# Performance work log

Hardware: AMD Instinct MI355X
Metric: run time of the kernel (lower is better)

## Reference

```python
import jax, jax.numpy as jnp
import numpy as np

B, CIN, COUT, H, W = 8, 256, 256, 64, 64


def setup_inputs() -> dict:
    key = jax.random.key(0)
    k1, k2, k3 = jax.random.split(key, 3)
    x = jax.random.normal(k1, (B, CIN, H, W), dtype=jnp.float32)
    style = jax.random.normal(k2, (B, CIN), dtype=jnp.float32)
    # kaiming_normal_ (fan_in = CIN*3*3, gain = sqrt(2))
    fan_in = CIN * 9
    weight = jax.random.normal(k3, (COUT, CIN, 3, 3), dtype=jnp.float32) * np.sqrt(2.0 / fan_in)
    return {"x": x, "style": style, "weight": weight}


def reference(x, style, weight):
    b, cin, h, w = x.shape
    cout = weight.shape[0]
    # modulate: [B, Cout, Cin, 3, 3]
    mw = style[:, None, :, None, None] * weight[None]
    # demodulate
    sigma = jnp.sqrt(jnp.sum(mw * mw, axis=(2, 3, 4), keepdims=True) + 1e-8)
    dw = mw / sigma
    # per-sample conv via grouped convolution (groups = B)
    x_g = x.reshape(1, b * cin, h, w)
    w_g = dw.reshape(b * cout, cin, 3, 3)
    out = jax.lax.conv_general_dilated(
        x_g, w_g,
        window_strides=(1, 1),
        padding=((1, 1), (1, 1)),
        feature_group_count=b,
        dimension_numbers=("NCHW", "OIHW", "NCHW"),
    )
    return out.reshape(b, cout, h, w)
```

## Files before the change

kernel.cpp:

```cpp
#include <hip/hip_runtime.h>

#define B_ 8
#define CIN_ 256
#define COUT_ 256

typedef short short8_t __attribute__((ext_vector_type(8)));
typedef float float16_t __attribute__((ext_vector_type(16)));

#define DWA_SHORTS   (B_ * 2 * 8 * 9 * 4 * 128 * 8)
#define XPRE_SHORTS  (B_ * 8 * 66 * 4 * 66 * 8)

__device__ __forceinline__ unsigned short f2bf(float f) {
    union { float f; unsigned u; } v; v.f = f;
    unsigned u = v.u;
    unsigned r = (u + 0x7fffu + ((u >> 16) & 1u)) >> 16;
    return (unsigned short)r;
}

__global__ __launch_bounds__(256) void k_prep(const float* __restrict__ x,
                                              const float* __restrict__ style,
                                              const float* __restrict__ weight,
                                              unsigned short* __restrict__ xpre,
                                              float* __restrict__ invp) {
    const int bid = blockIdx.x;
    const int t = threadIdx.x;

    if (bid < 4224) {
        const int h_out = bid % 66;
        const int t2 = bid / 66;
        const int cb = t2 & 7, b = t2 >> 3;
        const int h_in = h_out - 1;
        const int g = t >> 6, lane = t & 63;
        unsigned short* dst =
            xpre + (((size_t)(b * 8 + cb) * 66 + h_out) * 4 + g) * (66 * 8);
#pragma unroll
        for (int pass = 0; pass < 2; ++pass) {
            int w_out = pass * 64 + lane;
            if (pass == 1 && lane >= 2) break;
            int w_in = w_out - 1;
            short8_t v = (short8_t){0, 0, 0, 0, 0, 0, 0, 0};
            if ((unsigned)h_in < 64u && (unsigned)w_in < 64u) {
                const float* xp =
                    x + (((size_t)(b * CIN_ + cb * 32 + g * 8)) * 64 + h_in) * 64 + w_in;
#pragma unroll
                for (int j = 0; j < 8; ++j) v[j] = (short)f2bf(xp[(size_t)j * 4096]);
            }
            *(short8_t*)(dst + (size_t)w_out * 8) = v;
        }
    } else {
        const int co = (bid - 4224) * 16 + (t >> 4);
        const int sl = t & 15;
        float part[8];
#pragma unroll
        for (int b = 0; b < 8; ++b) part[b] = 0.f;
        const float* wr = weight + (size_t)co * 2304 + sl * 16 * 9;
#pragma unroll 4
        for (int k = 0; k < 16; ++k) {
            int ci = sl * 16 + k;
            float a = 0.f;
#pragma unroll
            for (int tp = 0; tp < 9; ++tp) { float w = wr[k * 9 + tp]; a += w * w; }
#pragma unroll
            for (int b = 0; b < 8; ++b) {
                float s = style[b * CIN_ + ci];
                part[b] += s * s * a;
            }
        }
#pragma unroll
        for (int b = 0; b < 8; ++b) {
            float p = part[b];
            p += __shfl_xor(p, 1, 64);
            p += __shfl_xor(p, 2, 64);
            p += __shfl_xor(p, 4, 64);
            p += __shfl_xor(p, 8, 64);
            if (sl == 0) invp[b * COUT_ + co] = 1.0f / sqrtf(p + 1e-8f);
        }
    }
}

__global__ __launch_bounds__(256) void k_wpack(const float* __restrict__ weight,
                                               const float* __restrict__ style,
                                               const float* __restrict__ invp,
                                               unsigned short* __restrict__ dwA) {
    const int co_blk = blockIdx.x, cb = blockIdx.y, b = blockIdx.z;
    const int t = threadIdx.x;
    unsigned short* slab = dwA + (((size_t)(b * 2 + co_blk) * 8 + cb) * 9) * 4096;
    const int co = co_blk * 128 + (t & 127);
    const float iv = invp[b * COUT_ + co];
    const float* wco = weight + (size_t)co * 2304;
#pragma unroll
    for (int i = 0; i < 18; ++i) {
        int o8 = t + i * 256;
        int g = (o8 >> 7) & 3;
        int tap = o8 >> 9;
        int ci0 = cb * 32 + g * 8;
        short8_t v;
#pragma unroll
        for (int k = 0; k < 8; ++k)
            v[k] = (short)f2bf(wco[(ci0 + k) * 9 + tap] * style[b * CIN_ + ci0 + k] * iv);
        *(short8_t*)(slab + (size_t)o8 * 8) = v;
    }
}

__global__ __launch_bounds__(256, 2) void k_conv(const unsigned short* __restrict__ xpre,
                                                 const unsigned short* __restrict__ dwA,
                                                 float* __restrict__ out) {
    __shared__ __align__(16) unsigned short xs[2][4 * 4 * 66 * 8];

    const int rowgrp = blockIdx.x;
    const int co_blk = blockIdx.y;
    const int b = blockIdx.z;
    const int tid = threadIdx.x;
    const int lane = tid & 63, wid = tid >> 6;
    const int wave_m = wid & 1;
    const int wave_r = wid >> 1;
    const int l32 = lane & 31, kh = lane >> 5;
    const int r0 = rowgrp * 2;

    float16_t acc[2][2];
#pragma unroll
    for (int mi = 0; mi < 2; ++mi)
#pragma unroll
        for (int nj = 0; nj < 2; ++nj)
#pragma unroll
            for (int r = 0; r < 16; ++r) acc[mi][nj][r] = 0.f;

    short8_t st[5];
    auto load_regs = [&](int cb) {
        const unsigned short* s =
            xpre + ((size_t)(b * 8 + cb) * 66 + r0) * (4 * 66 * 8);
#pragma unroll
        for (int it = 0; it < 4; ++it)
            st[it] = *(const short8_t*)(s + (size_t)(tid + it * 256) * 8);
        if (tid < 32) st[4] = *(const short8_t*)(s + (size_t)(tid + 1024) * 8);
    };
    auto store_lds = [&](int buf) {
        unsigned short* d = xs[buf];
#pragma unroll
        for (int it = 0; it < 4; ++it)
            *(short8_t*)(d + (size_t)(tid + it * 256) * 8) = st[it];
        if (tid < 32) *(short8_t*)(d + (size_t)(tid + 1024) * 8) = st[4];
    };

    short8_t abuf[3][4];
    auto loadA = [&](short8_t* dst, int acb, int atap) {
        const unsigned short* Ab =
            dwA + ((((size_t)(b * 2 + co_blk) * 8 + acb) * 9 + atap)) * 4096;
        const int co_off = wave_m * 64 + l32;
#pragma unroll
        for (int ks = 0; ks < 2; ++ks)
#pragma unroll
            for (int mi = 0; mi < 2; ++mi)
                dst[ks * 2 + mi] = *(const short8_t*)(
                    Ab + (size_t)((ks * 2 + kh) * 128 + co_off + mi * 32) * 8);
    };

    load_regs(0);
    loadA(abuf[0], 0, 0);
    loadA(abuf[1], 0, 1);

    for (int cb = 0; cb < 8; ++cb) {
        store_lds(cb & 1);
        __syncthreads();
        if (cb < 7) load_regs(cb + 1);

        const unsigned short* xb = xs[cb & 1];
#pragma unroll
        for (int tap = 0; tap < 9; ++tap) {
            const int nl = tap + 2;
            const int acb = cb + nl / 9, atap = nl % 9;
            if (acb < 8) loadA(abuf[(tap + 2) % 3], acb, atap);

            const int dh = tap / 3, dwc = tap - dh * 3;
            const unsigned short* bb =
                xb + (size_t)(((wave_r + dh) * 4 + kh) * 66 + l32 + dwc) * 8;
            short8_t bf[2][2];
#pragma unroll
            for (int ks = 0; ks < 2; ++ks)
#pragma unroll
                for (int nj = 0; nj < 2; ++nj)
                    bf[ks][nj] = *(const short8_t*)(bb + (size_t)(ks * 2 * 66 + nj * 32) * 8);

            const short8_t* ac = abuf[tap % 3];
#pragma unroll
            for (int ks = 0; ks < 2; ++ks)
#pragma unroll
                for (int mi = 0; mi < 2; ++mi)
#pragma unroll
                    for (int nj = 0; nj < 2; ++nj)
                        acc[mi][nj] = __builtin_amdgcn_mfma_f32_32x32x16_bf16(
                            ac[ks * 2 + mi], bf[ks][nj], acc[mi][nj], 0, 0, 0);
        }
    }

    const int orow = r0 + wave_r;
#pragma unroll
    for (int mi = 0; mi < 2; ++mi)
#pragma unroll
        for (int nj = 0; nj < 2; ++nj)
#pragma unroll
            for (int r = 0; r < 16; ++r) {
                int co = co_blk * 128 + wave_m * 64 + mi * 32 + (r & 3) + 8 * (r >> 2) + 4 * kh;
                int c = nj * 32 + l32;
                out[(((size_t)b * COUT_ + co) * 64 + orow) * 64 + c] = acc[mi][nj][r];
            }
}

extern "C" void kernel_launch(void* const* d_in, const int* in_sizes, int n_in,
                              void* d_out, int out_size, void* d_ws, size_t ws_size,
                              hipStream_t stream) {
    const float* x = (const float*)d_in[0];
    const float* style = (const float*)d_in[1];
    const float* weight = (const float*)d_in[2];
    float* out = (float*)d_out;

    unsigned short* dwA = (unsigned short*)d_ws;
    unsigned short* xpre = dwA + DWA_SHORTS;
    float* invp = (float*)(xpre + XPRE_SHORTS);

    k_prep<<<dim3(4240), 256, 0, stream>>>(x, style, weight, xpre, invp);
    k_wpack<<<dim3(2, 8, B_), 256, 0, stream>>>(weight, style, invp, dwA);
    k_conv<<<dim3(32, 2, B_), 256, 0, stream>>>(xpre, dwA, out);
}
```

Measured before the change: 152.8 us.

## Fuse demodulation into weight packing and shrink conv tile to one row

Merges the weight demodulation and the weight packing into the prep kernel. Each of 64 extra blocks computes the inverse sigma for 32 output channels of one sample into shared memory, then packs its slice of the bf16 weights, which removes one kernel launch and the invp round trip. The conv kernel now handles one output row per block with waves split across columns, so it launches twice as many blocks, uses less LDS and fewer accumulators, and allows 4 blocks per CU. In exchange each block reloads the A weights for half the output work, which raises weight traffic per FLOP.

```diff
diff --git a/kernel.cpp b/kernel.cpp
--- a/kernel.cpp
+++ b/kernel.cpp
@@ -21,7 +21,7 @@
                                               const float* __restrict__ style,
                                               const float* __restrict__ weight,
                                               unsigned short* __restrict__ xpre,
-                                              float* __restrict__ invp) {
+                                              unsigned short* __restrict__ dwA) {
     const int bid = blockIdx.x;
     const int t = threadIdx.x;
 
@@ -48,104 +48,94 @@
             *(short8_t*)(dst + (size_t)w_out * 8) = v;
         }
     } else {
-        const int co = (bid - 4224) * 16 + (t >> 4);
-        const int sl = t & 15;
-        float part[8];
-#pragma unroll
-        for (int b = 0; b < 8; ++b) part[b] = 0.f;
-        const float* wr = weight + (size_t)co * 2304 + sl * 16 * 9;
+        __shared__ float sinv[32];
+        const int j = bid - 4224;
+        const int b = j >> 3, grp = j & 7;
+
+        const int co_l = t >> 3, cpart = t & 7;
+        const int co = grp * 32 + co_l;
+        const float* wco = weight + (size_t)co * 2304;
+        float acc = 0.f;
 #pragma unroll 4
-        for (int k = 0; k < 16; ++k) {
-            int ci = sl * 16 + k;
+        for (int c2 = 0; c2 < 32; ++c2) {
+            int ci = cpart * 32 + c2;
             float a = 0.f;
 #pragma unroll
-            for (int tp = 0; tp < 9; ++tp) { float w = wr[k * 9 + tp]; a += w * w; }
-#pragma unroll
-            for (int b = 0; b < 8; ++b) {
-                float s = style[b * CIN_ + ci];
-                part[b] += s * s * a;
-            }
-        }
-#pragma unroll
-        for (int b = 0; b < 8; ++b) {
-            float p = part[b];
-            p += __shfl_xor(p, 1, 64);
-            p += __shfl_xor(p, 2, 64);
-            p += __shfl_xor(p, 4, 64);
-            p += __shfl_xor(p, 8, 64);
-            if (sl == 0) invp[b * COUT_ + co] = 1.0f / sqrtf(p + 1e-8f);
+            for (int tp = 0; tp < 9; ++tp) { float w = wco[ci * 9 + tp]; a += w * w; }
+            float s = style[b * CIN_ + ci];
+            acc += s * s * a;
+        }
+        acc += __shfl_xor(acc, 1, 64);
+        acc += __shfl_xor(acc, 2, 64);
+        acc += __shfl_xor(acc, 4, 64);
+        if (cpart == 0) sinv[co_l] = 1.0f / sqrtf(acc + 1e-8f);
+        __syncthreads();
+
+        const int co_blk = grp >> 2;
+#pragma unroll 4
+        for (int i = 0; i < 36; ++i) {
+            int c = t + i * 256;
+            int cb = c / 1152;
+            int r = c - cb * 1152;
+            int tap = r >> 7;
+            int r2 = r & 127;
+            int g = r2 >> 5, co32 = r2 & 31;
+            int coo = grp * 32 + co32;
+            int co128 = (grp & 3) * 32 + co32;
+            int ci0 = cb * 32 + g * 8;
+            const float iv = sinv[co32];
+            const float* wp = weight + (size_t)coo * 2304;
+            short8_t v;
+#pragma unroll
+            for (int k = 0; k < 8; ++k)
+                v[k] = (short)f2bf(wp[(ci0 + k) * 9 + tap] * style[b * CIN_ + ci0 + k] * iv);
+            unsigned short* slab =
+                dwA + (((size_t)(b * 2 + co_blk) * 8 + cb) * 9 + tap) * 4096;
+            *(short8_t*)(slab + (size_t)(g * 128 + co128) * 8) = v;
         }
     }
 }
 
-__global__ __launch_bounds__(256) void k_wpack(const float* __restrict__ weight,
-                                               const float* __restrict__ style,
-                                               const float* __restrict__ invp,
-                                               unsigned short* __restrict__ dwA) {
-    const int co_blk = blockIdx.x, cb = blockIdx.y, b = blockIdx.z;
-    const int t = threadIdx.x;
-    unsigned short* slab = dwA + (((size_t)(b * 2 + co_blk) * 8 + cb) * 9) * 4096;
-    const int co = co_blk * 128 + (t & 127);
-    const float iv = invp[b * COUT_ + co];
-    const float* wco = weight + (size_t)co * 2304;
-#pragma unroll
-    for (int i = 0; i < 18; ++i) {
-        int o8 = t + i * 256;
-        int g = (o8 >> 7) & 3;
-        int tap = o8 >> 9;
-        int ci0 = cb * 32 + g * 8;
-        short8_t v;
-#pragma unroll
-        for (int k = 0; k < 8; ++k)
-            v[k] = (short)f2bf(wco[(ci0 + k) * 9 + tap] * style[b * CIN_ + ci0 + k] * iv);
-        *(short8_t*)(slab + (size_t)o8 * 8) = v;
-    }
-}
-
-__global__ __launch_bounds__(256, 2) void k_conv(const unsigned short* __restrict__ xpre,
+__global__ __launch_bounds__(256, 4) void k_conv(const unsigned short* __restrict__ xpre,
                                                  const unsigned short* __restrict__ dwA,
                                                  float* __restrict__ out) {
-    __shared__ __align__(16) unsigned short xs[2][4 * 4 * 66 * 8];
-
-    const int rowgrp = blockIdx.x;
+    __shared__ __align__(16) unsigned short xs[2][3 * 4 * 66 * 8];
+
+    const int row = blockIdx.x;
     const int co_blk = blockIdx.y;
     const int b = blockIdx.z;
     const int tid = threadIdx.x;
     const int lane = tid & 63, wid = tid >> 6;
     const int wave_m = wid & 1;
-    const int wave_r = wid >> 1;
+    const int wave_n = wid >> 1;
     const int l32 = lane & 31, kh = lane >> 5;
-    const int r0 = rowgrp * 2;
-
-    float16_t acc[2][2];
+
+    float16_t acc[2];
 #pragma unroll
     for (int mi = 0; mi < 2; ++mi)
 #pragma unroll
-        for (int nj = 0; nj < 2; ++nj)
-#pragma unroll
-            for (int r = 0; r < 16; ++r) acc[mi][nj][r] = 0.f;
-
-    short8_t st[5];
+        for (int r = 0; r < 16; ++r) acc[mi][r] = 0.f;
+
+    short8_t st[4];
     auto load_regs = [&](int cb) {
-        const unsigned short* s =
-            xpre + ((size_t)(b * 8 + cb) * 66 + r0) * (4 * 66 * 8);
-#pragma unroll
-        for (int it = 0; it < 4; ++it)
+        const unsigned short* s = xpre + ((size_t)(b * 8 + cb) * 66 + row) * 2112;
+#pragma unroll
+        for (int it = 0; it < 3; ++it)
             st[it] = *(const short8_t*)(s + (size_t)(tid + it * 256) * 8);
-        if (tid < 32) st[4] = *(const short8_t*)(s + (size_t)(tid + 1024) * 8);
+        if (tid < 24) st[3] = *(const short8_t*)(s + (size_t)(tid + 768) * 8);
     };
     auto store_lds = [&](int buf) {
         unsigned short* d = xs[buf];
 #pragma unroll
-        for (int it = 0; it < 4; ++it)
+        for (int it = 0; it < 3; ++it)
             *(short8_t*)(d + (size_t)(tid + it * 256) * 8) = st[it];
-        if (tid < 32) *(short8_t*)(d + (size_t)(tid + 1024) * 8) = st[4];
+        if (tid < 24) *(short8_t*)(d + (size_t)(tid + 768) * 8) = st[3];
     };
 
     short8_t abuf[3][4];
     auto loadA = [&](short8_t* dst, int acb, int atap) {
         const unsigned short* Ab =
-            dwA + ((((size_t)(b * 2 + co_blk) * 8 + acb) * 9 + atap)) * 4096;
+            dwA + (((size_t)(b * 2 + co_blk) * 8 + acb) * 9 + atap) * 4096;
         const int co_off = wave_m * 64 + l32;
 #pragma unroll
         for (int ks = 0; ks < 2; ++ks)
@@ -173,37 +163,30 @@
 
             const int dh = tap / 3, dwc = tap - dh * 3;
             const unsigned short* bb =
-                xb + (size_t)(((wave_r + dh) * 4 + kh) * 66 + l32 + dwc) * 8;
-            short8_t bf[2][2];
+                xb + (size_t)((dh * 4 + kh) * 66 + wave_n * 32 + l32 + dwc) * 8;
+            short8_t bf[2];
 #pragma unroll
             for (int ks = 0; ks < 2; ++ks)
-#pragma unroll
-                for (int nj = 0; nj < 2; ++nj)
-                    bf[ks][nj] = *(const short8_t*)(bb + (size_t)(ks * 2 * 66 + nj * 32) * 8);
+                bf[ks] = *(const short8_t*)(bb + (size_t)(ks * 2 * 66) * 8);
 
             const short8_t* ac = abuf[tap % 3];
 #pragma unroll
             for (int ks = 0; ks < 2; ++ks)
 #pragma unroll
                 for (int mi = 0; mi < 2; ++mi)
-#pragma unroll
-                    for (int nj = 0; nj < 2; ++nj)
-                        acc[mi][nj] = __builtin_amdgcn_mfma_f32_32x32x16_bf16(
-                            ac[ks * 2 + mi], bf[ks][nj], acc[mi][nj], 0, 0, 0);
+                    acc[mi] = __builtin_amdgcn_mfma_f32_32x32x16_bf16(
+                        ac[ks * 2 + mi], bf[ks], acc[mi], 0, 0, 0);
         }
     }
 
-    const int orow = r0 + wave_r;
+    const int col = wave_n * 32 + l32;
 #pragma unroll
     for (int mi = 0; mi < 2; ++mi)
 #pragma unroll
-        for (int nj = 0; nj < 2; ++nj)
-#pragma unroll
-            for (int r = 0; r < 16; ++r) {
-                int co = co_blk * 128 + wave_m * 64 + mi * 32 + (r & 3) + 8 * (r >> 2) + 4 * kh;
-                int c = nj * 32 + l32;
-                out[(((size_t)b * COUT_ + co) * 64 + orow) * 64 + c] = acc[mi][nj][r];
-            }
+        for (int r = 0; r < 16; ++r) {
+            int co = co_blk * 128 + wave_m * 64 + mi * 32 + (r & 3) + 8 * (r >> 2) + 4 * kh;
+            out[(((size_t)b * COUT_ + co) * 64 + row) * 64 + col] = acc[mi][r];
+        }
 }
 
 extern "C" void kernel_launch(void* const* d_in, const int* in_sizes, int n_in,
@@ -216,9 +199,7 @@
 
     unsigned short* dwA = (unsigned short*)d_ws;
     unsigned short* xpre = dwA + DWA_SHORTS;
-    float* invp = (float*)(xpre + XPRE_SHORTS);
-
-    k_prep<<<dim3(4240), 256, 0, stream>>>(x, style, weight, xpre, invp);
-    k_wpack<<<dim3(2, 8, B_), 256, 0, stream>>>(weight, style, invp, dwA);
-    k_conv<<<dim3(32, 2, B_), 256, 0, stream>>>(xpre, dwA, out);
-}
+
+    k_prep<<<dim3(4288), 256, 0, stream>>>(x, style, weight, xpre, dwA);
+    k_conv<<<dim3(64, 2, B_), 256, 0, stream>>>(xpre, dwA, out);
+}
```

New measurement: 223.2 us. 1.46x slower.
